# Optimization experiments

Hardware: AMD Instinct MI355X
Metric: run time of the kernel (lower is better)

## Reference

```python
import jax, jax.numpy as jnp
import numpy as np

N_LAYERS = 2
D = 128


def _prelu(z, a):
    return jnp.where(z >= 0, z, a * z)


def _seg_sum(vals, idx, num):
    return jax.ops.segment_sum(vals, idx, num_segments=num)


def _conv_layer(x, ni, ei, Wn2e, bn2e, We2n, be2n, alpha, Dn_inv, De_inv, num_nodes, num_edges):
    # node -> edge: mean over member nodes (row norm), then linear + bias + PReLU
    e = _seg_sum((x @ Wn2e)[ni] * De_inv[ei][:, None], ei, num_edges) + bn2e
    e = _prelu(e, alpha)
    # edge -> node: mean over incident hyperedges
    n = _seg_sum((e @ We2n)[ei] * Dn_inv[ni][:, None], ni, num_nodes) + be2n
    return n, e


def _encoder(x, ni, ei, Wn2e, bn2e, We2n, be2n, alpha, Dn_inv, De_inv, num_nodes, num_edges):
    e = None
    for i in range(N_LAYERS):
        x, e = _conv_layer(x, ni, ei, Wn2e[i], bn2e[i], We2n[i], be2n[i], alpha, Dn_inv, De_inv, num_nodes, num_edges)
        x = _prelu(x, alpha)
    return x, e


def _decoder(x, e, ni, ei, We, Wx, b, alpha, Dn_inv, num_nodes):
    for i in range(N_LAYERS):
        m = _seg_sum((e @ We[i])[ei] * Dn_inv[ni][:, None], ni, num_nodes)
        x = _prelu(x @ Wx[i] + m + b[i], alpha)
    return x


def _forward(x, xx,
             e1_Wn2e, e1_bn2e, e1_We2n, e1_be2n,
             e2_Wn2e, e2_bn2e, e2_We2n, e2_be2n,
             d1_We, d1_Wx, d1_b, d2_We, d2_Wx, d2_b,
             alpha, node_idx, edge_idx, num_nodes, num_edges):
    # self loops: each node gets its own private hyperedge (id num_edges + node_id)
    ni = jnp.concatenate([node_idx, jnp.arange(num_nodes, dtype=node_idx.dtype)])
    ei = jnp.concatenate([edge_idx, jnp.arange(num_edges, num_edges + num_nodes, dtype=edge_idx.dtype)])
    ne_tot = num_edges + num_nodes
    ones = jnp.ones(ni.shape[0], x.dtype)
    Dn = _seg_sum(ones, ni, num_nodes)
    De = _seg_sum(ones, ei, ne_tot)
    Dn_inv = jnp.where(Dn > 0, 1.0 / Dn, 0.0)
    De_inv = jnp.where(De > 0, 1.0 / De, 0.0)

    n1, e1 = _encoder(x, ni, ei, e1_Wn2e, e1_bn2e, e1_We2n, e1_be2n, alpha, Dn_inv, De_inv, num_nodes, ne_tot)
    n2, e2 = _encoder(xx, ni, ei, e2_Wn2e, e2_bn2e, e2_We2n, e2_be2n, alpha, Dn_inv, De_inv, num_nodes, ne_tot)

    x11 = _decoder(n1, e1, ni, ei, d1_We, d1_Wx, d1_b, alpha, Dn_inv, num_nodes)
    x21 = _decoder(n2, e2, ni, ei, d2_We, d2_Wx, d2_b, alpha, Dn_inv, num_nodes)
    x12 = _decoder(n2, e2, ni, ei, d1_We, d1_Wx, d1_b, alpha, Dn_inv, num_nodes)
    x22 = _decoder(n1, e1, ni, ei, d2_We, d2_Wx, d2_b, alpha, Dn_inv, num_nodes)

    nn1 = jnp.concatenate([n1, n2], axis=1)
    return (nn1, n1, e1[:num_edges], n2, e2[:num_edges], x11, x21, x12, x22)


def setup_inputs() -> dict:
    key = jax.random.key(0)
    ks = jax.random.split(key, 24)
    N, E, NNZ = 50000, 20000, 800000
    s = 1.0 / np.sqrt(D)
    inp = {
        'x': jax.random.normal(ks[0], (N, D), jnp.float32),
        'xx': jax.random.normal(ks[1], (N, D), jnp.float32),
        'node_idx': jax.random.randint(ks[2], (NNZ,), 0, N, jnp.int32),
        'edge_idx': jax.random.randint(ks[3], (NNZ,), 0, E, jnp.int32),
        'num_nodes': N,
        'num_edges': E,
        'alpha': jnp.float32(0.25),
    }
    i = 4
    for enc in ('e1', 'e2'):
        inp[enc + '_Wn2e'] = jax.random.normal(ks[i], (N_LAYERS, D, D), jnp.float32) * s; i += 1
        inp[enc + '_bn2e'] = jnp.zeros((N_LAYERS, D), jnp.float32)
        inp[enc + '_We2n'] = jax.random.normal(ks[i], (N_LAYERS, D, D), jnp.float32) * s; i += 1
        inp[enc + '_be2n'] = jnp.zeros((N_LAYERS, D), jnp.float32)
    for dec in ('d1', 'd2'):
        inp[dec + '_We'] = jax.random.normal(ks[i], (N_LAYERS, D, D), jnp.float32) * s; i += 1
        inp[dec + '_Wx'] = jax.random.normal(ks[i], (N_LAYERS, D, D), jnp.float32) * s; i += 1
        inp[dec + '_b'] = jnp.zeros((N_LAYERS, D), jnp.float32)
    return inp


def reference(x, xx,
              e1_Wn2e, e1_bn2e, e1_We2n, e1_be2n,
              e2_Wn2e, e2_bn2e, e2_We2n, e2_be2n,
              d1_We, d1_Wx, d1_b, d2_We, d2_Wx, d2_b,
              alpha, node_idx, edge_idx, num_nodes, num_edges):
    return _forward(x, xx,
                    e1_Wn2e, e1_bn2e, e1_We2n, e1_be2n,
                    e2_Wn2e, e2_bn2e, e2_We2n, e2_be2n,
                    d1_We, d1_Wx, d1_b, d2_We, d2_Wx, d2_b,
                    alpha, node_idx, edge_idx, num_nodes, num_edges)
```

## Files before the change

kernel.cpp:

```cpp
#include <hip/hip_runtime.h>

#define DD 128

typedef __attribute__((ext_vector_type(8))) short bh8;
typedef __attribute__((ext_vector_type(8))) unsigned short us8;
typedef __attribute__((ext_vector_type(4))) unsigned short us4;
typedef __attribute__((ext_vector_type(4))) float f4;
typedef unsigned int u32;
typedef unsigned short u16;

__device__ __forceinline__ u16 tob(float f) {
  u32 u = __builtin_bit_cast(u32, f);
  u += 0x7FFFu + ((u >> 16) & 1u);
  return (u16)(u >> 16);
}
__device__ __forceinline__ float fb(u16 h) { return __builtin_bit_cast(float, (u32)h << 16); }


__global__ __launch_bounds__(256) void init_counts_k(int* cn, int* ce, int N, int E) {
  int g = blockIdx.x * blockDim.x + threadIdx.x;
  if (g < E) ce[g] = 0;
  if (g < N) cn[g] = 0;
}

__global__ __launch_bounds__(256) void hist_k(const int* __restrict__ ni, const int* __restrict__ ei,
                                              int* cn, int* ce, int nnz) {
  int stride = gridDim.x * blockDim.x;
  for (int j = blockIdx.x * blockDim.x + threadIdx.x; j < nnz; j += stride) {
    atomicAdd(&cn[ni[j]], 1);
    atomicAdd(&ce[ei[j]], 1);
  }
}


__global__ __launch_bounds__(256) void scan_partials_k(const int* __restrict__ cn, const int* __restrict__ ce,
                                                       int* part, int NCHN, int N, int NCHE, int E) {
  __shared__ int red[256];
  int b = blockIdx.x, tid = threadIdx.x;
  const int* cnt = (b < NCHN) ? cn : ce;
  int n = (b < NCHN) ? N : E;
  int base = ((b < NCHN) ? b : (b - NCHN)) << 10;
  int i0 = base + tid * 4;
  int s = 0;
  #pragma unroll
  for (int j = 0; j < 4; ++j) { int i = i0 + j; if (i < n) s += cnt[i]; }
  red[tid] = s; __syncthreads();
  for (int off = 128; off > 0; off >>= 1) {
    if (tid < off) red[tid] += red[tid + off];
    __syncthreads();
  }
  if (tid == 0) part[b] = red[0];
}

__device__ __forceinline__ int blk_excl_scan(int s, int tid, int* sums) {
  sums[tid] = s; __syncthreads();
  for (int off = 1; off < 256; off <<= 1) {
    int t = (tid >= off) ? sums[tid - off] : 0;
    __syncthreads();
    sums[tid] += t;
    __syncthreads();
  }
  int ex = sums[tid] - s;
  __syncthreads();
  return ex;
}

__global__ __launch_bounds__(256) void scan_chunks_k(int* part, int NCHN, int NCHE) {
  __shared__ int sums[256];
  int tid = threadIdx.x;
  {
    int v = (tid < NCHN) ? part[tid] : 0;
    int ex = blk_excl_scan(v, tid, sums);
    if (tid < NCHN) part[tid] = ex;
  }
  __syncthreads();
  {
    int v = (tid < NCHE) ? part[NCHN + tid] : 0;
    int ex = blk_excl_scan(v, tid, sums);
    if (tid < NCHE) part[NCHN + tid] = ex;
  }
}

__global__ __launch_bounds__(256) void scan_apply_k(const int* __restrict__ cn, const int* __restrict__ ce,
                                                    const int* __restrict__ part,
                                                    int* offs_n, int* offs_e,
                                                    int NCHN, int N, int NCHE, int E) {
  __shared__ int sums[256];
  int b = blockIdx.x, tid = threadIdx.x;
  const int* cnt = (b < NCHN) ? cn : ce;
  int* offs = (b < NCHN) ? offs_n : offs_e;
  int n = (b < NCHN) ? N : E;
  int base = ((b < NCHN) ? b : (b - NCHN)) << 10;
  int i0 = base + tid * 4;
  int v[4]; int s = 0;
  #pragma unroll
  for (int j = 0; j < 4; ++j) { int i = i0 + j; int t = (i < n) ? cnt[i] : 0; v[j] = t; s += t; }
  int ex = blk_excl_scan(s, tid, sums);
  int run = part[b] + ex;
  #pragma unroll
  for (int j = 0; j < 4; ++j) { int i = i0 + j; if (i < n) offs[i] = run; run += v[j]; }
  if (tid == 255 && base + 1024 >= n) offs[n] = run;
}

__global__ __launch_bounds__(256) void fill_deg_k(const int* __restrict__ offs_n, const int* __restrict__ offs_e,
                                                  float* Dn_inv, float* De_inv,
                                                  int* cur_be, int* cur_bn, int* cur_n, int* cur_e,
                                                  int N, int E, int NBE, int NBN) {
  int g = blockIdx.x * blockDim.x + threadIdx.x;
  if (g < E) {
    int b = offs_e[g], e = offs_e[g + 1];
    De_inv[g] = (e > b) ? 1.0f / (float)(e - b) : 0.0f;
    cur_e[g] = b;
  }
  if (g < N) {
    int b = offs_n[g], e = offs_n[g + 1];
    Dn_inv[g] = 1.0f / (float)(e - b + 1);
    cur_n[g] = b;
  }
  if (g < NBE) {
    int r1 = (g + 1) * 32; if (r1 > E) r1 = E;
    int o0 = offs_e[g * 32], o1 = offs_e[r1];
    int C = o1 - o0, base = 8 * o0;
    #pragma unroll
    for (int k = 0; k < 8; ++k) cur_be[g * 8 + k] = base + k * C;
  }
  if (g < NBN) {
    int r1 = (g + 1) * 32; if (r1 > N) r1 = N;
    int o0 = offs_n[g * 32], o1 = offs_n[r1];
    int C = o1 - o0, base = 8 * o0;
    #pragma unroll
    for (int k = 0; k < 8; ++k) cur_bn[g * 8 + k] = base + k * C;
  }
}

__global__ __launch_bounds__(256) void partition2_k(const int* __restrict__ ni, const int* __restrict__ ei,
                                                    int* cur_be, int* cur_bn,
                                                    u32* __restrict__ SE, u32* __restrict__ SN, int nnz) {
  int xcd;
  asm volatile("s_getreg_b32 %0, hwreg(HW_REG_XCC_ID)" : "=s"(xcd));
  xcd &= 7;
  int stride = gridDim.x * blockDim.x;
  for (int j = blockIdx.x * blockDim.x + threadIdx.x; j < nnz; j += stride) {
    int n = ni[j], e = ei[j];
    int pe = atomicAdd(&cur_be[(e >> 5) * 8 + xcd], 1);
    SE[pe] = ((u32)(e & 31) << 17) | (u32)n;
    int pn = atomicAdd(&cur_bn[(n >> 5) * 8 + xcd], 1);
    SN[pn] = ((u32)(n & 31) << 17) | (u32)e;
  }
}

__global__ __launch_bounds__(256) void scatter2_k(const u32* __restrict__ S, const int* __restrict__ offs,
                                                  const int* __restrict__ cur_b,
                                                  int* __restrict__ list, int nRows) {
  __shared__ int cur[32];
  const int b = blockIdx.x;
  const int i0 = b << 5;
  const int tid = threadIdx.x;
  if (tid < 32) {
    int row = i0 + tid;
    cur[tid] = (row < nRows) ? offs[row] : 0;
  }
  __syncthreads();
  int r1 = i0 + 32; if (r1 > nRows) r1 = nRows;
  const int o0 = offs[i0];
  const int C = offs[r1] - o0;
  #pragma unroll 1
  for (int k = 0; k < 8; ++k) {
    int sbeg = 8 * o0 + k * C;
    int send = cur_b[b * 8 + k];
    for (int i = sbeg + tid; i < send; i += 256) {
      u32 v = S[i];
      int pos = atomicAdd(&cur[v >> 17], 1);
      list[pos] = (int)(v & 0x1FFFFu);
    }
  }
}

__global__ __launch_bounds__(256) void fill_nnz_k(const int* __restrict__ ni, const int* __restrict__ ei,
                                                  int* cur_n, int* cur_e, int* listN, int* listE, int nnz) {
  int stride = gridDim.x * blockDim.x;
  for (int j = blockIdx.x * blockDim.x + threadIdx.x; j < nnz; j += stride) {
    int n = ni[j], e = ei[j];
    int pn = atomicAdd(&cur_n[n], 1); listN[pn] = e;
    int pe = atomicAdd(&cur_e[e], 1); listE[pe] = n;
  }
}


__device__ __forceinline__ void acc4(float4& a, us4 v) {
  a.x += fb(v[0]); a.y += fb(v[1]); a.z += fb(v[2]); a.w += fb(v[3]);
}

template<int SPLIT>
__global__ __launch_bounds__(256) void gather_edge_k(const u16* __restrict__ srcb,
                                                     const int* __restrict__ offs, const int* __restrict__ list,
                                                     const float* __restrict__ De_inv,
                                                     const float* __restrict__ b1, const float* __restrict__ b2,
                                                     const float* __restrict__ alphap,
                                                     u16* __restrict__ e_fullb,
                                                     float* __restrict__ d2a, float* __restrict__ d2b, int E) {
  const int wave = threadIdx.x >> 6, lane = threadIdx.x & 63;
  const int row = blockIdx.x * 4 + wave;
  if (row >= E) return;
  const int c = lane * 4;
  const int beg = offs[row], end = offs[row + 1];
  float4 a0 = {0,0,0,0}, a1 = {0,0,0,0}, a2 = {0,0,0,0}, a3 = {0,0,0,0};
  int i = beg;
  for (; i + 3 < end; i += 4) {
    int s0 = list[i], s1 = list[i + 1], s2 = list[i + 2], s3 = list[i + 3];
    us4 v0 = *(const us4*)&srcb[(size_t)s0 * 256 + c];
    us4 v1 = *(const us4*)&srcb[(size_t)s1 * 256 + c];
    us4 v2 = *(const us4*)&srcb[(size_t)s2 * 256 + c];
    us4 v3 = *(const us4*)&srcb[(size_t)s3 * 256 + c];
    acc4(a0, v0); acc4(a1, v1); acc4(a2, v2); acc4(a3, v3);
  }
  for (; i < end; ++i) acc4(a0, *(const us4*)&srcb[(size_t)list[i] * 256 + c]);
  float sc = De_inv[row];
  const float* bp = (c < 128) ? (b1 + c) : (b2 + c - 128);
  float4 bt = *(const float4*)bp;
  float al = *alphap;
  float4 o;
  o.x = sc * ((a0.x + a1.x) + (a2.x + a3.x)) + bt.x;
  o.y = sc * ((a0.y + a1.y) + (a2.y + a3.y)) + bt.y;
  o.z = sc * ((a0.z + a1.z) + (a2.z + a3.z)) + bt.z;
  o.w = sc * ((a0.w + a1.w) + (a2.w + a3.w)) + bt.w;
  o.x = (o.x >= 0.f) ? o.x : al * o.x;
  o.y = (o.y >= 0.f) ? o.y : al * o.y;
  o.z = (o.z >= 0.f) ? o.z : al * o.z;
  o.w = (o.w >= 0.f) ? o.w : al * o.w;
  us4 ob = {tob(o.x), tob(o.y), tob(o.z), tob(o.w)};
  *(us4*)&e_fullb[(size_t)row * 256 + c] = ob;
  if constexpr (SPLIT == 1) {
    if (c < 128) *(float4*)&d2a[(size_t)row * DD + c] = o;
    else         *(float4*)&d2b[(size_t)row * DD + c - 128] = o;
  }
}

__global__ __launch_bounds__(256) void gather_node_k(const u16* __restrict__ e_fullb,
                                                     const u16* __restrict__ tb,
                                                     const int* __restrict__ offs, const int* __restrict__ list,
                                                     const float* __restrict__ Dn_inv,
                                                     const float* __restrict__ b1, const float* __restrict__ b2,
                                                     const float* __restrict__ alphap,
                                                     u16* __restrict__ dstb, int N) {
  const int wave = threadIdx.x >> 6, lane = threadIdx.x & 63;
  const int row = blockIdx.x * 4 + wave;
  if (row >= N) return;
  const int c = lane * 4;
  const int beg = offs[row], end = offs[row + 1];
  float4 a0 = {0,0,0,0}, a1 = {0,0,0,0}, a2 = {0,0,0,0}, a3 = {0,0,0,0};
  int i = beg;
  for (; i + 3 < end; i += 4) {
    int s0 = list[i], s1 = list[i + 1], s2 = list[i + 2], s3 = list[i + 3];
    us4 v0 = *(const us4*)&e_fullb[(size_t)s0 * 256 + c];
    us4 v1 = *(const us4*)&e_fullb[(size_t)s1 * 256 + c];
    us4 v2 = *(const us4*)&e_fullb[(size_t)s2 * 256 + c];
    us4 v3 = *(const us4*)&e_fullb[(size_t)s3 * 256 + c];
    acc4(a0, v0); acc4(a1, v1); acc4(a2, v2); acc4(a3, v3);
  }
  for (; i < end; ++i) acc4(a0, *(const us4*)&e_fullb[(size_t)list[i] * 256 + c]);
  us4 tv4 = *(const us4*)&tb[(size_t)row * 256 + c];
  const float* bp = (c < 128) ? (b1 + c) : (b2 + c - 128);
  float4 bt = *(const float4*)bp;
  float al = *alphap;
  float sx = fb(tv4[0]) + bt.x; sx = (sx >= 0.f) ? sx : al * sx;
  float sy = fb(tv4[1]) + bt.y; sy = (sy >= 0.f) ? sy : al * sy;
  float sz = fb(tv4[2]) + bt.z; sz = (sz >= 0.f) ? sz : al * sz;
  float sw = fb(tv4[3]) + bt.w; sw = (sw >= 0.f) ? sw : al * sw;
  float sc = Dn_inv[row];
  us4 ob;
  ob[0] = tob(sc * (sx + ((a0.x + a1.x) + (a2.x + a3.x))));
  ob[1] = tob(sc * (sy + ((a0.y + a1.y) + (a2.y + a3.y))));
  ob[2] = tob(sc * (sz + ((a0.z + a1.z) + (a2.z + a3.z))));
  ob[3] = tob(sc * (sw + ((a0.w + a1.w) + (a2.w + a3.w))));
  *(us4*)&dstb[(size_t)row * 256 + c] = ob;
}


struct WPtrs { const float* p[16]; };

__global__ __launch_bounds__(256) void prep_w_k(WPtrs wp, char* dst) {
  int m = blockIdx.x >> 3, s = blockIdx.x & 7;
  const float* W = wp.p[m];
  int t = threadIdx.x;
  int n = t & 127;
  int k0 = s * 16 + (t >> 7) * 8;
  us8 vhi, vlo;
  #pragma unroll
  for (int j = 0; j < 8; ++j) {
    float x = W[(size_t)(k0 + j) * DD + n];
    u32 ux = __builtin_bit_cast(u32, x);
    float hf = __builtin_bit_cast(float, ux & 0xFFFF0000u);
    float l = x - hf;
    vhi[j] = (u16)(ux >> 16);
    vlo[j] = (u16)(__builtin_bit_cast(u32, l) >> 16);
  }
  char* base = dst + (size_t)m * 65536;
  int byte = n * 256 + k0 * 2;
  byte ^= (n & 7) << 4;
  *(us8*)(base + byte) = vhi;
  *(us8*)(base + 32768 + byte) = vlo;
}


__device__ __forceinline__ void stage_w(const char* gsrc, char* lds, int tid) {
  int wave = tid >> 6, lane = tid & 63;
  #pragma unroll
  for (int i = 0; i < 16; ++i) {
    int off = (wave * 16 + i) * 1024;
    __builtin_amdgcn_global_load_lds(
        (const __attribute__((address_space(1))) u32*)(gsrc + off + lane * 16),
        (__attribute__((address_space(3))) u32*)(lds + off), 16, 0, 0);
  }
}

__device__ __forceinline__ void split8(const float vs[8], bh8& hi, bh8& lo) {
  #pragma unroll
  for (int j = 0; j < 8; ++j) {
    u32 u = __builtin_bit_cast(u32, vs[j]);
    float hf = __builtin_bit_cast(float, u & 0xFFFF0000u);
    float l = vs[j] - hf;
    hi[j] = (short)(u >> 16);
    lo[j] = (short)(__builtin_bit_cast(u32, l) >> 16);
  }
}

__device__ __forceinline__ void mk_afrag(const float* rowp, int koff, bh8& hi, bh8& lo) {
  float4 v0 = *(const float4*)(rowp + koff);
  float4 v1 = *(const float4*)(rowp + koff + 4);
  float vs[8] = {v0.x, v0.y, v0.z, v0.w, v1.x, v1.y, v1.z, v1.w};
  split8(vs, hi, lo);
}

__device__ __forceinline__ void mfma_ks(const bh8& ahi, const bh8& alo, const char* Wl,
                                        int ks, int lane, f4 acc[8]) {
  const int koff0 = (lane >> 4) * 8;
  const int k2 = (ks * 32 + koff0) * 2;
  #pragma unroll
  for (int cb = 0; cb < 8; ++cb) {
    int n = cb * 16 + (lane & 15);
    int byte = (n * 256 + k2) ^ ((n & 7) << 4);
    bh8 bhiF = *(const bh8*)(Wl + byte);
    bh8 bloF = *(const bh8*)(Wl + 32768 + byte);
    acc[cb] = __builtin_amdgcn_mfma_f32_16x16x32_bf16(ahi, bhiF, acc[cb], 0, 0, 0);
    acc[cb] = __builtin_amdgcn_mfma_f32_16x16x32_bf16(ahi, bloF, acc[cb], 0, 0, 0);
    acc[cb] = __builtin_amdgcn_mfma_f32_16x16x32_bf16(alo, bhiF, acc[cb], 0, 0, 0);
  }
}

__device__ __forceinline__ void mfma_ks_bf(const bh8& a, const char* Wl,
                                           int ks, int lane, f4 acc[8]) {
  const int koff0 = (lane >> 4) * 8;
  const int k2 = (ks * 32 + koff0) * 2;
  #pragma unroll
  for (int cb = 0; cb < 8; ++cb) {
    int n = cb * 16 + (lane & 15);
    int byte = (n * 256 + k2) ^ ((n & 7) << 4);
    bh8 bhiF = *(const bh8*)(Wl + byte);
    bh8 bloF = *(const bh8*)(Wl + 32768 + byte);
    acc[cb] = __builtin_amdgcn_mfma_f32_16x16x32_bf16(a, bhiF, acc[cb], 0, 0, 0);
    acc[cb] = __builtin_amdgcn_mfma_f32_16x16x32_bf16(a, bloF, acc[cb], 0, 0, 0);
  }
}

__device__ __forceinline__ void mfma_passS(const float* __restrict__ A, size_t astride, int acoff,
                                           const char* Wl, int rbase, int nrows, int lane, f4 acc[8]) {
  int r = rbase + (lane & 15);
  if (r >= nrows) r = nrows - 1;
  const float* rowp = A + (size_t)r * astride + acoff;
  const int koff0 = (lane >> 4) * 8;
  #pragma unroll
  for (int ks = 0; ks < 4; ++ks) {
    bh8 ahi, alo;
    mk_afrag(rowp, ks * 32 + koff0, ahi, alo);
    mfma_ks(ahi, alo, Wl, ks, lane, acc);
  }
}

__device__ __forceinline__ void mfma_passB(const u16* __restrict__ A, size_t astride, int acoff,
                                           const char* Wl, int rbase, int nrows, int lane, f4 acc[8]) {
  int r = rbase + (lane & 15);
  if (r >= nrows) r = nrows - 1;
  const u16* rowp = A + (size_t)r * astride + acoff;
  const int koff0 = (lane >> 4) * 8;
  #pragma unroll
  for (int ks = 0; ks < 4; ++ks) {
    bh8 a = __builtin_bit_cast(bh8, *(const us8*)(rowp + ks * 32 + koff0));
    mfma_ks_bf(a, Wl, ks, lane, acc);
  }
}

struct AFragB { bh8 a[4]; };

__device__ __forceinline__ void load_afragB(const u16* __restrict__ A, size_t astride, int acoff,
                                            int rbase, int nrows, int lane, AFragB& f) {
  int r = rbase + (lane & 15);
  if (r >= nrows) r = nrows - 1;
  const u16* rowp = A + (size_t)r * astride + acoff;
  const int koff0 = (lane >> 4) * 8;
  #pragma unroll
  for (int ks = 0; ks < 4; ++ks)
    f.a[ks] = __builtin_bit_cast(bh8, *(const us8*)(rowp + ks * 32 + koff0));
}

__device__ __forceinline__ void mfma_pass_fragB(const AFragB& f, const char* Wl, int lane, f4 acc[8]) {
  #pragma unroll
  for (int ks = 0; ks < 4; ++ks) mfma_ks_bf(f.a[ks], Wl, ks, lane, acc);
}


__device__ __forceinline__ void acc_to_T(f4 acc[8], const float* bias, float al,
                                         char* Tb, int wave, int lane) {
  const int cidx = lane & 15;
  float b8[8];
  #pragma unroll
  for (int cb = 0; cb < 8; ++cb) b8[cb] = bias[cb * 16 + cidx];
  #pragma unroll
  for (int q = 0; q < 4; ++q) {
    int row = wave * 16 + (lane >> 4) * 4 + q;
    #pragma unroll
    for (int cb = 0; cb < 8; ++cb) {
      float v = acc[cb][q] + b8[cb];
      v = (v >= 0.f) ? v : al * v;
      int byte = (row * 256 + (cb * 16 + cidx) * 2) ^ ((row & 7) << 4);
      *(u16*)(Tb + byte) = tob(v);
    }
  }
}

__device__ __forceinline__ void load_fT(const char* Tb, int wave, int lane, AFragB& f) {
  const int row = wave * 16 + (lane & 15);
  const int koff0 = (lane >> 4) * 8;
  #pragma unroll
  for (int ks = 0; ks < 4; ++ks) {
    int byte = (row * 256 + (ks * 32 + koff0) * 2) ^ ((row & 7) << 4);
    f.a[ks] = __builtin_bit_cast(bh8, *(const us8*)(Tb + byte));
  }
}

template<int MODE, int OBF>
__device__ __forceinline__ void epilogueS(f4 acc[8], const float* bias, const float* alphap,
                                          void* outp, size_t ostride, int ocoff,
                                          int rbase, int nrows, int lane) {
  float al = 0.f;
  if constexpr (MODE == 1) al = *alphap;
  const int cidx = lane & 15;
  int rq = rbase + (lane >> 4) * 4;
  float b8[8];
  if constexpr (MODE == 1) {
    #pragma unroll
    for (int cb = 0; cb < 8; ++cb) b8[cb] = bias[cb * 16 + cidx];
  }
  #pragma unroll
  for (int q = 0; q < 4; ++q) {
    int row = rq + q;
    if (row < nrows) {
      #pragma unroll
      for (int cb = 0; cb < 8; ++cb) {
        float v = acc[cb][q];
        if constexpr (MODE == 1) { v += b8[cb]; v = (v >= 0.f) ? v : al * v; }
        if constexpr (OBF == 1) {
          u16* op = (u16*)outp + (size_t)row * ostride + ocoff + cidx;
          op[cb * 16] = tob(v);
        } else {
          float* op = (float*)outp + (size_t)row * ostride + ocoff + cidx;
          op[cb * 16] = v;
        }
      }
    }
  }
}

#define ACC_ZERO(acc) { _Pragma("unroll") for (int cb = 0; cb < 8; ++cb) acc[cb] = {0.f, 0.f, 0.f, 0.f}; }


template<int MODE, int OBF, int ABF>
__global__ __launch_bounds__(256, 2) void gemm_halves_k(const void* __restrict__ A1, size_t as1, int ac1, const char* W1, const float* b1_,
                                                        const void* __restrict__ A2, size_t as2, int ac2, const char* W2, const float* b2_,
                                                        const float* __restrict__ alphap,
                                                        void* __restrict__ out, int nrows) {
  __shared__ char Wl[65536];
  const int wave = threadIdx.x >> 6, lane = threadIdx.x & 63;
  const int rbase = blockIdx.x * 64 + wave * 16;
  f4 acc[8];
  stage_w(W1, Wl, threadIdx.x);
  __syncthreads();
  ACC_ZERO(acc);
  if constexpr (ABF) mfma_passB((const u16*)A1, as1, ac1, Wl, rbase, nrows, lane, acc);
  else               mfma_passS((const float*)A1, as1, ac1, Wl, rbase, nrows, lane, acc);
  epilogueS<MODE, OBF>(acc, b1_, alphap, out, 256, 0, rbase, nrows, lane);
  __syncthreads();
  stage_w(W2, Wl, threadIdx.x);
  __syncthreads();
  ACC_ZERO(acc);
  if constexpr (ABF) mfma_passB((const u16*)A2, as2, ac2, Wl, rbase, nrows, lane, acc);
  else               mfma_passS((const float*)A2, as2, ac2, Wl, rbase, nrows, lane, acc);
  epilogueS<MODE, OBF>(acc, b2_, alphap, out, 256, 128, rbase, nrows, lane);
}

__global__ __launch_bounds__(256, 2) void gemm_fuse_hid_k(const u16* __restrict__ thb,
                                                          const char* W20, const float* b20, const char* W21,
                                                          const char* W60, const float* b60, const char* W61,
                                                          const float* __restrict__ alphap,
                                                          u16* __restrict__ tb_out, int nrows) {
  __shared__ char Wl[65536];
  const int wave = threadIdx.x >> 6, lane = threadIdx.x & 63;
  const int rbase = blockIdx.x * 64 + wave * 16;
  const float al = *alphap;
  f4 acc[8];
  AFragB fT;
  #pragma unroll 1
  for (int h = 0; h < 2; ++h) {
    if (h) __syncthreads();
    stage_w(h ? W60 : W20, Wl, threadIdx.x);
    __syncthreads();
    ACC_ZERO(acc);
    mfma_passB(thb, 256, h * 128, Wl, rbase, nrows, lane, acc);
    __syncthreads();
    acc_to_T(acc, h ? b60 : b20, al, Wl, wave, lane);
    __syncthreads();
    load_fT(Wl, wave, lane, fT);
    __syncthreads();
    stage_w(h ? W61 : W21, Wl, threadIdx.x);
    __syncthreads();
    ACC_ZERO(acc);
    mfma_pass_fragB(fT, Wl, lane, acc);
    epilogueS<0, 1>(acc, nullptr, nullptr, tb_out, 256, h * 128, rbase, nrows, lane);
  }
}

__global__ __launch_bounds__(256, 2) void enc_final_k(const u16* __restrict__ aggb, const char* W1, const float* b1_,
                                                      const char* W2, const float* b2_,
                                                      const float* __restrict__ alphap,
                                                      float* __restrict__ n1, float* __restrict__ n2,
                                                      u16* __restrict__ n1b, u16* __restrict__ n2b,
                                                      float* __restrict__ nn1, int nrows) {
  __shared__ char Wl[65536];
  const int wave = threadIdx.x >> 6, lane = threadIdx.x & 63;
  const int rbase = blockIdx.x * 64 + wave * 16;
  const int cidx = lane & 15;
  f4 acc[8];
  float al = *alphap;
  #pragma unroll 1
  for (int h = 0; h < 2; ++h) {
    if (h) __syncthreads();
    stage_w(h ? W2 : W1, Wl, threadIdx.x);
    __syncthreads();
    const float* bp = h ? b2_ : b1_;
    float* nout = h ? n2 : n1;
    u16* nbout = h ? n2b : n1b;
    float b8[8];
    #pragma unroll
    for (int cb = 0; cb < 8; ++cb) b8[cb] = bp[cb * 16 + cidx];
    ACC_ZERO(acc);
    mfma_passB(aggb, 256, h * 128, Wl, rbase, nrows, lane, acc);
    int rq = rbase + (lane >> 4) * 4;
    #pragma unroll
    for (int q = 0; q < 4; ++q) {
      int row = rq + q;
      if (row < nrows) {
        float* op = nout + (size_t)row * DD + cidx;
        float* op2 = nn1 + (size_t)row * 256 + h * 128 + cidx;
        u16* op3 = nbout + (size_t)row * DD + cidx;
        #pragma unroll
        for (int cb = 0; cb < 8; ++cb) {
          float v = acc[cb][q] + b8[cb];
          v = (v >= 0.f) ? v : al * v;
          op[cb * 16] = v;
          op2[cb * 16] = v;
          op3[cb * 16] = tob(v);
        }
      }
    }
  }
}

__global__ __launch_bounds__(256, 2) void dec_fused_k(const u16* __restrict__ n1b, const u16* __restrict__ n2b,
                                                      const u16* __restrict__ aggb,
                                                      const char* Wx10, const char* We10, const float* b1_0,
                                                      const char* Wx11, const char* We11, const float* b1_1,
                                                      const char* Wx20, const char* We20, const float* b2_0,
                                                      const char* Wx21, const char* We21, const float* b2_1,
                                                      const float* __restrict__ alphap,
                                                      float* __restrict__ x11, float* __restrict__ x22,
                                                      float* __restrict__ x12, float* __restrict__ x21,
                                                      int nrows) {
  __shared__ char Wl[65536];
  const int y = blockIdx.y;
  const u16* xb = y ? n2b : n1b;
  float* od1 = y ? x12 : x11;
  float* od2 = y ? x21 : x22;
  const int acoff = y * 128;
  const int wave = threadIdx.x >> 6, lane = threadIdx.x & 63;
  const int rbase = blockIdx.x * 64 + wave * 16;
  const float al = *alphap;
  AFragB fx, fa, fT;
  load_afragB(xb, DD, 0, rbase, nrows, lane, fx);
  load_afragB(aggb, 256, acoff, rbase, nrows, lane, fa);
  f4 acc[8];
  #pragma unroll 1
  for (int s = 0; s < 2; ++s) {
    const char* Wx0 = s ? Wx20 : Wx10;
    const char* We0 = s ? We20 : We10;
    const char* Wx1 = s ? Wx21 : Wx11;
    const char* We1 = s ? We21 : We11;
    const float* b0 = s ? b2_0 : b1_0;
    const float* b1 = s ? b2_1 : b1_1;
    float* out = s ? od2 : od1;
    if (s) __syncthreads();
    stage_w(Wx0, Wl, threadIdx.x);
    __syncthreads();
    ACC_ZERO(acc);
    mfma_pass_fragB(fx, Wl, lane, acc);
    __syncthreads();
    stage_w(We0, Wl, threadIdx.x);
    __syncthreads();
    mfma_pass_fragB(fa, Wl, lane, acc);
    __syncthreads();
    acc_to_T(acc, b0, al, Wl, wave, lane);
    __syncthreads();
    load_fT(Wl, wave, lane, fT);
    __syncthreads();
    stage_w(Wx1, Wl, threadIdx.x);
    __syncthreads();
    ACC_ZERO(acc);
    mfma_pass_fragB(fT, Wl, lane, acc);
    __syncthreads();
    stage_w(We1, Wl, threadIdx.x);
    __syncthreads();
    mfma_pass_fragB(fa, Wl, lane, acc);
    epilogueS<1, 0>(acc, b1, alphap, out, DD, 0, rbase, nrows, lane);
  }
}


extern "C" void kernel_launch(void* const* d_in, const int* in_sizes, int n_in,
                              void* d_out, int out_size, void* d_ws, size_t ws_size,
                              hipStream_t stream) {
  const float* x        = (const float*)d_in[0];
  const float* xx       = (const float*)d_in[1];
  const int*   node_idx = (const int*)d_in[2];
  const int*   edge_idx = (const int*)d_in[3];
  const float* alphap   = (const float*)d_in[6];
  const float* e1_Wn2e  = (const float*)d_in[7];
  const float* e1_bn2e  = (const float*)d_in[8];
  const float* e1_We2n  = (const float*)d_in[9];
  const float* e1_be2n  = (const float*)d_in[10];
  const float* e2_Wn2e  = (const float*)d_in[11];
  const float* e2_bn2e  = (const float*)d_in[12];
  const float* e2_We2n  = (const float*)d_in[13];
  const float* e2_be2n  = (const float*)d_in[14];
  const float* d1_We    = (const float*)d_in[15];
  const float* d1_Wx    = (const float*)d_in[16];
  const float* d1_b     = (const float*)d_in[17];
  const float* d2_We    = (const float*)d_in[18];
  const float* d2_Wx    = (const float*)d_in[19];
  const float* d2_b     = (const float*)d_in[20];

  const int N   = in_sizes[0] / DD;
  const int NNZ = in_sizes[2];
  const int E   = (out_size - 1024 * N) / 256;
  const int NBE = (E + 31) >> 5;
  const int NBN = (N + 31) >> 5;
  const int NCHN = (N + 1023) >> 10;
  const int NCHE = (E + 1023) >> 10;

  float* out  = (float*)d_out;
  float* nn1  = out;
  float* n1   = out + (size_t)N * 256;
  float* e1o  = n1 + (size_t)N * DD;
  float* n2   = e1o + (size_t)E * DD;
  float* e2o  = n2 + (size_t)N * DD;
  float* x11  = e2o + (size_t)E * DD;
  float* x21  = x11 + (size_t)N * DD;
  float* x12  = x21 + (size_t)N * DD;
  float* x22  = x12 + (size_t)N * DD;

  size_t off = 0;
  char* w0 = (char*)d_ws;
  auto carve = [&](size_t bytes) -> void* {
    void* p = (void*)(w0 + off);
    off += (bytes + 255) & ~(size_t)255;
    return p;
  };
  int* cn      = (int*)carve((size_t)N * 4);
  int* ce      = (int*)carve((size_t)E * 4);
  int* offs_n  = (int*)carve((size_t)(N + 1) * 4);
  int* offs_e  = (int*)carve((size_t)(E + 1) * 4);
  int* part    = (int*)carve((size_t)(NCHN + NCHE) * 4);
  int* listN   = (int*)carve((size_t)NNZ * 4);
  int* listE   = (int*)carve((size_t)NNZ * 4);
  float* Dn_inv = (float*)carve((size_t)N * 4);
  float* De_inv = (float*)carve((size_t)E * 4);
  char* Wprep  = (char*)carve((size_t)16 * 65536);
  u16* tb      = (u16*)carve((size_t)N * 256 * 2);
  u16* e_fullb = (u16*)carve((size_t)E * 256 * 2);
  u16* thb     = (u16*)carve((size_t)N * 256 * 2);
  u16* aggb    = (u16*)carve((size_t)N * 256 * 2);
  u16* n1b     = (u16*)carve((size_t)N * DD * 2);
  u16* n2b     = (u16*)carve((size_t)N * DD * 2);
  int* cur_n   = (int*)carve((size_t)N * 4);
  int* cur_e   = (int*)carve((size_t)E * 4);
  int* cur_be  = (int*)carve((size_t)NBE * 8 * 4);
  int* cur_bn  = (int*)carve((size_t)NBN * 8 * 4);
  u32* SE      = (u32*)carve((size_t)NNZ * 8 * 4);
  u32* SN      = (u32*)carve((size_t)NNZ * 8 * 4);
  const bool staged = off <= ws_size;

  WPtrs wp;
  wp.p[0] = e1_Wn2e;  wp.p[1] = e1_Wn2e + DD * DD;
  wp.p[2] = e1_We2n;  wp.p[3] = e1_We2n + DD * DD;
  wp.p[4] = e2_Wn2e;  wp.p[5] = e2_Wn2e + DD * DD;
  wp.p[6] = e2_We2n;  wp.p[7] = e2_We2n + DD * DD;
  wp.p[8] = d1_We;    wp.p[9] = d1_We + DD * DD;
  wp.p[10] = d1_Wx;   wp.p[11] = d1_Wx + DD * DD;
  wp.p[12] = d2_We;   wp.p[13] = d2_We + DD * DD;
  wp.p[14] = d2_Wx;   wp.p[15] = d2_Wx + DD * DD;
  auto WP = [&](int i) -> const char* { return Wprep + (size_t)i * 65536; };

  const int thr = 256;
  const int gMax = ((N > E ? N : E) + thr - 1) / thr;
  int gNNZ = (NNZ + thr - 1) / thr; if (gNNZ > 2048) gNNZ = 2048;
  const int NT = (N + 63) / 64;
  const int gGatE = (E + 3) / 4;
  const int gGatN = (N + 3) / 4;

  prep_w_k<<<128, 256, 0, stream>>>(wp, Wprep);
  init_counts_k<<<gMax, thr, 0, stream>>>(cn, ce, N, E);
  hist_k<<<gNNZ, thr, 0, stream>>>(node_idx, edge_idx, cn, ce, NNZ);
  scan_partials_k<<<NCHN + NCHE, 256, 0, stream>>>(cn, ce, part, NCHN, N, NCHE, E);
  scan_chunks_k<<<1, 256, 0, stream>>>(part, NCHN, NCHE);
  scan_apply_k<<<NCHN + NCHE, 256, 0, stream>>>(cn, ce, part, offs_n, offs_e, NCHN, N, NCHE, E);
  fill_deg_k<<<gMax, thr, 0, stream>>>(offs_n, offs_e, Dn_inv, De_inv,
                                       cur_be, cur_bn, cur_n, cur_e, N, E, NBE, NBN);

  if (staged) {
    partition2_k<<<gNNZ, thr, 0, stream>>>(node_idx, edge_idx, cur_be, cur_bn, SE, SN, NNZ);
    scatter2_k<<<NBE, 256, 0, stream>>>(SE, offs_e, cur_be, listE, E);
    scatter2_k<<<NBN, 256, 0, stream>>>(SN, offs_n, cur_bn, listN, N);
  } else {
    fill_nnz_k<<<gNNZ, thr, 0, stream>>>(node_idx, edge_idx, cur_n, cur_e, listN, listE, NNZ);
  }

  gemm_halves_k<0, 1, 0><<<NT, 256, 0, stream>>>(x, DD, 0, WP(0), nullptr,
                                                 xx, DD, 0, WP(4), nullptr, alphap, tb, N);
  gather_edge_k<0><<<gGatE, 256, 0, stream>>>(tb, offs_e, listE, De_inv, e1_bn2e, e2_bn2e,
                                              alphap, e_fullb, nullptr, nullptr, E);
  gather_node_k<<<gGatN, 256, 0, stream>>>(e_fullb, tb, offs_n, listN, Dn_inv, e1_bn2e, e2_bn2e,
                                           alphap, thb, N);
  gemm_fuse_hid_k<<<NT, 256, 0, stream>>>(thb, WP(2), e1_be2n, WP(1),
                                          WP(6), e2_be2n, WP(5), alphap, tb, N);
  gather_edge_k<1><<<gGatE, 256, 0, stream>>>(tb, offs_e, listE, De_inv, e1_bn2e + DD, e2_bn2e + DD,
                                              alphap, e_fullb, e1o, e2o, E);
  gather_node_k<<<gGatN, 256, 0, stream>>>(e_fullb, tb, offs_n, listN, Dn_inv, e1_bn2e + DD, e2_bn2e + DD,
                                           alphap, aggb, N);
  enc_final_k<<<NT, 256, 0, stream>>>(aggb, WP(3), e1_be2n + DD, WP(7), e2_be2n + DD,
                                      alphap, n1, n2, n1b, n2b, nn1, N);

  dim3 gDec(NT, 2);
  dec_fused_k<<<gDec, 256, 0, stream>>>(n1b, n2b, aggb,
                                        WP(10), WP(8), d1_b, WP(11), WP(9), d1_b + DD,
                                        WP(14), WP(12), d2_b, WP(15), WP(13), d2_b + DD,
                                        alphap, x11, x22, x12, x21, N);
}
```

Measured before the change: 609.3 us.

## Overlap histogram with first GEMM, merge scatters, widen gather loads

```diff
diff --git a/kernel.cpp b/kernel.cpp
--- a/kernel.cpp
+++ b/kernel.cpp
@@ -21,15 +21,6 @@
   int g = blockIdx.x * blockDim.x + threadIdx.x;
   if (g < E) ce[g] = 0;
   if (g < N) cn[g] = 0;
-}
-
-__global__ __launch_bounds__(256) void hist_k(const int* __restrict__ ni, const int* __restrict__ ei,
-                                              int* cn, int* ce, int nnz) {
-  int stride = gridDim.x * blockDim.x;
-  for (int j = blockIdx.x * blockDim.x + threadIdx.x; j < nnz; j += stride) {
-    atomicAdd(&cn[ni[j]], 1);
-    atomicAdd(&ce[ei[j]], 1);
-  }
 }
 
 
@@ -149,13 +140,10 @@
   }
 }
 
-__global__ __launch_bounds__(256) void scatter2_k(const u32* __restrict__ S, const int* __restrict__ offs,
-                                                  const int* __restrict__ cur_b,
-                                                  int* __restrict__ list, int nRows) {
-  __shared__ int cur[32];
-  const int b = blockIdx.x;
+__device__ __forceinline__ void scatter_body(const u32* __restrict__ S, const int* __restrict__ offs,
+                                             const int* __restrict__ cur_b,
+                                             int* __restrict__ list, int nRows, int b, int tid, int* cur) {
   const int i0 = b << 5;
-  const int tid = threadIdx.x;
   if (tid < 32) {
     int row = i0 + tid;
     cur[tid] = (row < nRows) ? offs[row] : 0;
@@ -176,19 +164,20 @@
   }
 }
 
-__global__ __launch_bounds__(256) void fill_nnz_k(const int* __restrict__ ni, const int* __restrict__ ei,
-                                                  int* cur_n, int* cur_e, int* listN, int* listE, int nnz) {
-  int stride = gridDim.x * blockDim.x;
-  for (int j = blockIdx.x * blockDim.x + threadIdx.x; j < nnz; j += stride) {
-    int n = ni[j], e = ei[j];
-    int pn = atomicAdd(&cur_n[n], 1); listN[pn] = e;
-    int pe = atomicAdd(&cur_e[e], 1); listE[pe] = n;
-  }
-}
-
-
-__device__ __forceinline__ void acc4(float4& a, us4 v) {
-  a.x += fb(v[0]); a.y += fb(v[1]); a.z += fb(v[2]); a.w += fb(v[3]);
+__global__ __launch_bounds__(256) void scatter_both_k(const u32* SE, const int* offs_e, const int* cur_be,
+                                                      int* listE, int E, int NBE,
+                                                      const u32* SN, const int* offs_n, const int* cur_bn,
+                                                      int* listN, int N) {
+  __shared__ int cur[32];
+  int b = blockIdx.x, tid = threadIdx.x;
+  if (b < NBE) scatter_body(SE, offs_e, cur_be, listE, E, b, tid, cur);
+  else         scatter_body(SN, offs_n, cur_bn, listN, N, b - NBE, tid, cur);
+}
+
+
+__device__ __forceinline__ void acc8(float a[8], us8 v) {
+  #pragma unroll
+  for (int j = 0; j < 8; ++j) a[j] += fb(v[j]);
 }
 
 template<int SPLIT>
@@ -202,37 +191,45 @@
   const int wave = threadIdx.x >> 6, lane = threadIdx.x & 63;
   const int row = blockIdx.x * 4 + wave;
   if (row >= E) return;
-  const int c = lane * 4;
+  const int half = lane >> 5, cl = lane & 31;
+  const int c8 = cl * 8;
   const int beg = offs[row], end = offs[row + 1];
-  float4 a0 = {0,0,0,0}, a1 = {0,0,0,0}, a2 = {0,0,0,0}, a3 = {0,0,0,0};
-  int i = beg;
-  for (; i + 3 < end; i += 4) {
-    int s0 = list[i], s1 = list[i + 1], s2 = list[i + 2], s3 = list[i + 3];
-    us4 v0 = *(const us4*)&srcb[(size_t)s0 * 256 + c];
-    us4 v1 = *(const us4*)&srcb[(size_t)s1 * 256 + c];
-    us4 v2 = *(const us4*)&srcb[(size_t)s2 * 256 + c];
-    us4 v3 = *(const us4*)&srcb[(size_t)s3 * 256 + c];
-    acc4(a0, v0); acc4(a1, v1); acc4(a2, v2); acc4(a3, v3);
-  }
-  for (; i < end; ++i) acc4(a0, *(const us4*)&srcb[(size_t)list[i] * 256 + c]);
-  float sc = De_inv[row];
-  const float* bp = (c < 128) ? (b1 + c) : (b2 + c - 128);
-  float4 bt = *(const float4*)bp;
-  float al = *alphap;
-  float4 o;
-  o.x = sc * ((a0.x + a1.x) + (a2.x + a3.x)) + bt.x;
-  o.y = sc * ((a0.y + a1.y) + (a2.y + a3.y)) + bt.y;
-  o.z = sc * ((a0.z + a1.z) + (a2.z + a3.z)) + bt.z;
-  o.w = sc * ((a0.w + a1.w) + (a2.w + a3.w)) + bt.w;
-  o.x = (o.x >= 0.f) ? o.x : al * o.x;
-  o.y = (o.y >= 0.f) ? o.y : al * o.y;
-  o.z = (o.z >= 0.f) ? o.z : al * o.z;
-  o.w = (o.w >= 0.f) ? o.w : al * o.w;
-  us4 ob = {tob(o.x), tob(o.y), tob(o.z), tob(o.w)};
-  *(us4*)&e_fullb[(size_t)row * 256 + c] = ob;
-  if constexpr (SPLIT == 1) {
-    if (c < 128) *(float4*)&d2a[(size_t)row * DD + c] = o;
-    else         *(float4*)&d2b[(size_t)row * DD + c - 128] = o;
+  float a0[8] = {0,0,0,0,0,0,0,0}, a1[8] = {0,0,0,0,0,0,0,0};
+  int i = beg + half;
+  for (; i + 2 < end; i += 4) {
+    us8 v0 = *(const us8*)&srcb[(size_t)list[i] * 256 + c8];
+    us8 v1 = *(const us8*)&srcb[(size_t)list[i + 2] * 256 + c8];
+    acc8(a0, v0); acc8(a1, v1);
+  }
+  if (i < end) acc8(a0, *(const us8*)&srcb[(size_t)list[i] * 256 + c8]);
+  float s[8];
+  #pragma unroll
+  for (int j = 0; j < 8; ++j) s[j] = a0[j] + a1[j];
+  #pragma unroll
+  for (int j = 0; j < 8; ++j) s[j] += __shfl_xor(s[j], 32);
+  if (half == 0) {
+    float sc = De_inv[row];
+    const float* bp = (c8 < 128) ? (b1 + c8) : (b2 + c8 - 128);
+    float4 bt0 = *(const float4*)bp;
+    float4 bt1 = *(const float4*)(bp + 4);
+    float bb[8] = {bt0.x, bt0.y, bt0.z, bt0.w, bt1.x, bt1.y, bt1.z, bt1.w};
+    float al = *alphap;
+    us8 ob;
+    float ov[8];
+    #pragma unroll
+    for (int j = 0; j < 8; ++j) {
+      float v = sc * s[j] + bb[j];
+      v = (v >= 0.f) ? v : al * v;
+      ov[j] = v; ob[j] = tob(v);
+    }
+    *(us8*)&e_fullb[(size_t)row * 256 + c8] = ob;
+    if constexpr (SPLIT == 1) {
+      float* dp = (c8 < 128) ? &d2a[(size_t)row * DD + c8] : &d2b[(size_t)row * DD + c8 - 128];
+      float4 w0 = {ov[0], ov[1], ov[2], ov[3]};
+      float4 w1 = {ov[4], ov[5], ov[6], ov[7]};
+      *(float4*)dp = w0;
+      *(float4*)(dp + 4) = w1;
+    }
   }
 }
 
@@ -246,34 +243,39 @@
   const int wave = threadIdx.x >> 6, lane = threadIdx.x & 63;
   const int row = blockIdx.x * 4 + wave;
   if (row >= N) return;
-  const int c = lane * 4;
+  const int half = lane >> 5, cl = lane & 31;
+  const int c8 = cl * 8;
   const int beg = offs[row], end = offs[row + 1];
-  float4 a0 = {0,0,0,0}, a1 = {0,0,0,0}, a2 = {0,0,0,0}, a3 = {0,0,0,0};
-  int i = beg;
-  for (; i + 3 < end; i += 4) {
-    int s0 = list[i], s1 = list[i + 1], s2 = list[i + 2], s3 = list[i + 3];
-    us4 v0 = *(const us4*)&e_fullb[(size_t)s0 * 256 + c];
-    us4 v1 = *(const us4*)&e_fullb[(size_t)s1 * 256 + c];
-    us4 v2 = *(const us4*)&e_fullb[(size_t)s2 * 256 + c];
-    us4 v3 = *(const us4*)&e_fullb[(size_t)s3 * 256 + c];
-    acc4(a0, v0); acc4(a1, v1); acc4(a2, v2); acc4(a3, v3);
-  }
-  for (; i < end; ++i) acc4(a0, *(const us4*)&e_fullb[(size_t)list[i] * 256 + c]);
-  us4 tv4 = *(const us4*)&tb[(size_t)row * 256 + c];
-  const float* bp = (c < 128) ? (b1 + c) : (b2 + c - 128);
-  float4 bt = *(const float4*)bp;
-  float al = *alphap;
-  float sx = fb(tv4[0]) + bt.x; sx = (sx >= 0.f) ? sx : al * sx;
-  float sy = fb(tv4[1]) + bt.y; sy = (sy >= 0.f) ? sy : al * sy;
-  float sz = fb(tv4[2]) + bt.z; sz = (sz >= 0.f) ? sz : al * sz;
-  float sw = fb(tv4[3]) + bt.w; sw = (sw >= 0.f) ? sw : al * sw;
-  float sc = Dn_inv[row];
-  us4 ob;
-  ob[0] = tob(sc * (sx + ((a0.x + a1.x) + (a2.x + a3.x))));
-  ob[1] = tob(sc * (sy + ((a0.y + a1.y) + (a2.y + a3.y))));
-  ob[2] = tob(sc * (sz + ((a0.z + a1.z) + (a2.z + a3.z))));
-  ob[3] = tob(sc * (sw + ((a0.w + a1.w) + (a2.w + a3.w))));
-  *(us4*)&dstb[(size_t)row * 256 + c] = ob;
+  float a0[8] = {0,0,0,0,0,0,0,0}, a1[8] = {0,0,0,0,0,0,0,0};
+  int i = beg + half;
+  for (; i + 2 < end; i += 4) {
+    us8 v0 = *(const us8*)&e_fullb[(size_t)list[i] * 256 + c8];
+    us8 v1 = *(const us8*)&e_fullb[(size_t)list[i + 2] * 256 + c8];
+    acc8(a0, v0); acc8(a1, v1);
+  }
+  if (i < end) acc8(a0, *(const us8*)&e_fullb[(size_t)list[i] * 256 + c8]);
+  float s[8];
+  #pragma unroll
+  for (int j = 0; j < 8; ++j) s[j] = a0[j] + a1[j];
+  #pragma unroll
+  for (int j = 0; j < 8; ++j) s[j] += __shfl_xor(s[j], 32);
+  if (half == 0) {
+    us8 tv = *(const us8*)&tb[(size_t)row * 256 + c8];
+    const float* bp = (c8 < 128) ? (b1 + c8) : (b2 + c8 - 128);
+    float4 bt0 = *(const float4*)bp;
+    float4 bt1 = *(const float4*)(bp + 4);
+    float bb[8] = {bt0.x, bt0.y, bt0.z, bt0.w, bt1.x, bt1.y, bt1.z, bt1.w};
+    float al = *alphap;
+    float sc = Dn_inv[row];
+    us8 ob;
+    #pragma unroll
+    for (int j = 0; j < 8; ++j) {
+      float sv = fb(tv[j]) + bb[j];
+      sv = (sv >= 0.f) ? sv : al * sv;
+      ob[j] = tob(sc * (sv + s[j]));
+    }
+    *(us8*)&dstb[(size_t)row * 256 + c8] = ob;
+  }
 }
 
 
@@ -474,28 +476,35 @@
 #define ACC_ZERO(acc) { _Pragma("unroll") for (int cb = 0; cb < 8; ++cb) acc[cb] = {0.f, 0.f, 0.f, 0.f}; }
 
 
-template<int MODE, int OBF, int ABF>
-__global__ __launch_bounds__(256, 2) void gemm_halves_k(const void* __restrict__ A1, size_t as1, int ac1, const char* W1, const float* b1_,
-                                                        const void* __restrict__ A2, size_t as2, int ac2, const char* W2, const float* b2_,
-                                                        const float* __restrict__ alphap,
-                                                        void* __restrict__ out, int nrows) {
+__global__ __launch_bounds__(256, 2) void combo1_k(const float* __restrict__ x, const char* W0,
+                                                   const float* __restrict__ xx, const char* W4,
+                                                   u16* __restrict__ tb, int nrows, int NT,
+                                                   const int* __restrict__ ni, const int* __restrict__ ei,
+                                                   int* cn, int* ce, int nnz) {
   __shared__ char Wl[65536];
-  const int wave = threadIdx.x >> 6, lane = threadIdx.x & 63;
-  const int rbase = blockIdx.x * 64 + wave * 16;
-  f4 acc[8];
-  stage_w(W1, Wl, threadIdx.x);
-  __syncthreads();
-  ACC_ZERO(acc);
-  if constexpr (ABF) mfma_passB((const u16*)A1, as1, ac1, Wl, rbase, nrows, lane, acc);
-  else               mfma_passS((const float*)A1, as1, ac1, Wl, rbase, nrows, lane, acc);
-  epilogueS<MODE, OBF>(acc, b1_, alphap, out, 256, 0, rbase, nrows, lane);
-  __syncthreads();
-  stage_w(W2, Wl, threadIdx.x);
-  __syncthreads();
-  ACC_ZERO(acc);
-  if constexpr (ABF) mfma_passB((const u16*)A2, as2, ac2, Wl, rbase, nrows, lane, acc);
-  else               mfma_passS((const float*)A2, as2, ac2, Wl, rbase, nrows, lane, acc);
-  epilogueS<MODE, OBF>(acc, b2_, alphap, out, 256, 128, rbase, nrows, lane);
+  if ((int)blockIdx.x < NT) {
+    const int wave = threadIdx.x >> 6, lane = threadIdx.x & 63;
+    const int rbase = blockIdx.x * 64 + wave * 16;
+    f4 acc[8];
+    stage_w(W0, Wl, threadIdx.x);
+    __syncthreads();
+    ACC_ZERO(acc);
+    mfma_passS(x, DD, 0, Wl, rbase, nrows, lane, acc);
+    epilogueS<0, 1>(acc, nullptr, nullptr, tb, 256, 0, rbase, nrows, lane);
+    __syncthreads();
+    stage_w(W4, Wl, threadIdx.x);
+    __syncthreads();
+    ACC_ZERO(acc);
+    mfma_passS(xx, DD, 0, Wl, rbase, nrows, lane, acc);
+    epilogueS<0, 1>(acc, nullptr, nullptr, tb, 256, 128, rbase, nrows, lane);
+  } else {
+    int nb = gridDim.x - NT;
+    int stride = nb * 256;
+    for (int j = ((int)blockIdx.x - NT) * 256 + (int)threadIdx.x; j < nnz; j += stride) {
+      atomicAdd(&cn[ni[j]], 1);
+      atomicAdd(&ce[ei[j]], 1);
+    }
+  }
 }
 
 __global__ __launch_bounds__(256, 2) void gemm_fuse_hid_k(const u16* __restrict__ thb,
@@ -705,7 +714,7 @@
   int* cur_bn  = (int*)carve((size_t)NBN * 8 * 4);
   u32* SE      = (u32*)carve((size_t)NNZ * 8 * 4);
   u32* SN      = (u32*)carve((size_t)NNZ * 8 * 4);
-  const bool staged = off <= ws_size;
+  (void)cur_n; (void)cur_e;
 
   WPtrs wp;
   wp.p[0] = e1_Wn2e;  wp.p[1] = e1_Wn2e + DD * DD;
@@ -720,30 +729,25 @@
 
   const int thr = 256;
   const int gMax = ((N > E ? N : E) + thr - 1) / thr;
+  const int NT = (N + 63) / 64;
+  const int HB = 512;
   int gNNZ = (NNZ + thr - 1) / thr; if (gNNZ > 2048) gNNZ = 2048;
-  const int NT = (N + 63) / 64;
   const int gGatE = (E + 3) / 4;
   const int gGatN = (N + 3) / 4;
 
   prep_w_k<<<128, 256, 0, stream>>>(wp, Wprep);
   init_counts_k<<<gMax, thr, 0, stream>>>(cn, ce, N, E);
-  hist_k<<<gNNZ, thr, 0, stream>>>(node_idx, edge_idx, cn, ce, NNZ);
+  combo1_k<<<NT + HB, 256, 0, stream>>>(x, WP(0), xx, WP(4), tb, N, NT,
+                                        node_idx, edge_idx, cn, ce, NNZ);
   scan_partials_k<<<NCHN + NCHE, 256, 0, stream>>>(cn, ce, part, NCHN, N, NCHE, E);
   scan_chunks_k<<<1, 256, 0, stream>>>(part, NCHN, NCHE);
   scan_apply_k<<<NCHN + NCHE, 256, 0, stream>>>(cn, ce, part, offs_n, offs_e, NCHN, N, NCHE, E);
   fill_deg_k<<<gMax, thr, 0, stream>>>(offs_n, offs_e, Dn_inv, De_inv,
                                        cur_be, cur_bn, cur_n, cur_e, N, E, NBE, NBN);
-
-  if (staged) {
-    partition2_k<<<gNNZ, thr, 0, stream>>>(node_idx, edge_idx, cur_be, cur_bn, SE, SN, NNZ);
-    scatter2_k<<<NBE, 256, 0, stream>>>(SE, offs_e, cur_be, listE, E);
-    scatter2_k<<<NBN, 256, 0, stream>>>(SN, offs_n, cur_bn, listN, N);
-  } else {
-    fill_nnz_k<<<gNNZ, thr, 0, stream>>>(node_idx, edge_idx, cur_n, cur_e, listN, listE, NNZ);
-  }
-
-  gemm_halves_k<0, 1, 0><<<NT, 256, 0, stream>>>(x, DD, 0, WP(0), nullptr,
-                                                 xx, DD, 0, WP(4), nullptr, alphap, tb, N);
+  partition2_k<<<gNNZ, thr, 0, stream>>>(node_idx, edge_idx, cur_be, cur_bn, SE, SN, NNZ);
+  scatter_both_k<<<NBE + NBN, 256, 0, stream>>>(SE, offs_e, cur_be, listE, E, NBE,
+                                                SN, offs_n, cur_bn, listN, N);
+
   gather_edge_k<0><<<gGatE, 256, 0, stream>>>(tb, offs_e, listE, De_inv, e1_bn2e, e2_bn2e,
                                               alphap, e_fullb, nullptr, nullptr, E);
   gather_node_k<<<gGatN, 256, 0, stream>>>(e_fullb, tb, offs_n, listN, Dn_inv, e1_bn2e, e2_bn2e,
```

After: 585.9 us. 1.04x faster.
